# Kernel optimization log

Hardware: AMD Instinct MI355X
Metric: run time of the kernel (lower is better)

The kernel has to match this reference:

```python
import jax, jax.numpy as jnp
import numpy as np
from math import pi

FC_IN, FC_OUT = 64, 64
LABEL_NC = 35
B, C, H, W = 2, 64, 128, 128
EPS = 1e-5
SLOPE = 0.01  # torch leaky_relu default


def _pa(h, w):
    # absolute normalized coordinates, matches init_pos buffers
    xs = (jnp.arange(h, dtype=jnp.float32) / h) * 2.0 - 1.0
    ys = (jnp.arange(w, dtype=jnp.float32) / w) * 2.0 - 1.0
    px = jnp.broadcast_to(xs[:, None], (h, w))
    py = jnp.broadcast_to(ys[None, :], (h, w))
    return jnp.stack([px, py], 0)  # (2,h,w)


def _coords(h, w):
    # f0=3; while-loop runs once (f=3 -> f=1), so exactly 4 channels
    f = 3.0
    ang_x = 2.0 * pi * jnp.remainder(jnp.arange(w, dtype=jnp.float32), f) / f
    ang_y = 2.0 * pi * jnp.remainder(jnp.arange(h, dtype=jnp.float32), f) / f
    xcos = jnp.broadcast_to(jnp.cos(ang_x)[None, :], (h, w))
    xsin = jnp.broadcast_to(jnp.sin(ang_x)[None, :], (h, w))
    ycos = jnp.broadcast_to(jnp.cos(ang_y)[:, None], (h, w))
    ysin = jnp.broadcast_to(jnp.sin(ang_y)[:, None], (h, w))
    return jnp.stack([xcos, xsin, ycos, ysin], 0)  # (4,h,w)


def _nearest(t, h, w):
    # F.interpolate(mode='nearest') index map: floor(i*in/out)
    ih = jnp.arange(h) * t.shape[2] // h
    iw = jnp.arange(w) * t.shape[3] // w
    return t[:, :, ih][:, :, :, iw]


def setup_inputs() -> dict:
    key = jax.random.key(0)
    ks = jax.random.split(key, 7)
    return {
        "x": jax.random.normal(ks[0], (B, C, H, W), jnp.float32),
        "layout": jax.random.normal(ks[1], (B, LABEL_NC, H, W), jnp.float32),
        "pr": jax.random.normal(ks[2], (B, 2, H, W), jnp.float32),
        "conv_w": jax.random.normal(ks[3], (1, 10), jnp.float32) * 0.02,
        "conv_b": jnp.zeros((1,), jnp.float32),
        "W_table": jax.random.normal(ks[4], (LABEL_NC, FC_IN * FC_OUT), jnp.float32),
        "b_table": jax.random.normal(ks[5], (LABEL_NC, FC_OUT), jnp.float32) * 0.02,
        "pl": jax.random.normal(ks[6], (2, H, W), jnp.float32),
    }


def reference(x, layout, pr, conv_w, conv_b, W_table, b_table, pl):
    b, c, h, w = x.shape
    pa = jnp.broadcast_to(_pa(h, w)[None], (b, 2, h, w))
    plb = jnp.broadcast_to(pl[None], (b, 2, h, w))
    coords = jnp.broadcast_to(_coords(h, w)[None], (b, 4, h, w))
    prr = _nearest(pr, h, w)
    pos = jnp.concatenate([pa, plb, prr, coords], axis=1)  # (B,10,h,w)
    # 1x1 conv to a single channel, broadcast-added over C
    x = x + jnp.einsum('bchw,oc->bohw', pos, conv_w) + conv_b[None, :, None, None]
    # argmax-routed per-pixel affine params
    lay = _nearest(layout, h, w)
    arg = jnp.argmax(lay, axis=1)  # (B,h,w) int
    Wg = W_table[arg].reshape(b, h, w, FC_IN, FC_OUT)  # huge gathered tensor (as in original)
    bg = b_table[arg]  # (B,h,w,FC_OUT)
    xh = jnp.transpose(x, (0, 2, 3, 1))  # (B,h,w,C)
    y = jnp.einsum('bhwc,bhwco->bhwo', xh, Wg) + bg
    y = jnp.transpose(y, (0, 3, 1, 2))  # (B,FC_OUT,h,w)
    # instance norm (no affine, biased variance, eps=1e-5)
    mu = jnp.mean(y, axis=(2, 3), keepdims=True)
    var = jnp.var(y, axis=(2, 3), keepdims=True)
    y = (y - mu) * jax.lax.rsqrt(var + EPS)
    return jnp.where(y >= 0, y, SLOPE * y)
```

## Files before the change

kernel.cpp:

```cpp
#include <hip/hip_runtime.h>

#define HH 128
#define WW 128
#define NPIX (HH*WW)
#define NC 35
#define NB1 512
#define NWIN 16
#define NGB (NC*NWIN)
#define NG (2*NGB)

__global__ __launch_bounds__(256) void prep_kernel(
    const float* __restrict__ x, const float* __restrict__ layout,
    const float* __restrict__ pr, const float* __restrict__ cw,
    const float* __restrict__ cb, const float* __restrict__ pl,
    float* __restrict__ xt, int* __restrict__ argbuf)
{
    __shared__ float s_t[64*65];
    __shared__ float s_s[64];

    const int t  = threadIdx.x;
    const int bk = blockIdx.x;
    const int b  = bk >> 8;
    const int p0 = (bk & 255) << 6;
    const int h  = p0 >> 7;
    const int w0 = p0 & 127;

    const float4* x4 = (const float4*)x + (size_t)b*64*4096 + (p0 >> 2);
    #pragma unroll
    for (int k = 0; k < 4; ++k) {
        int f = k*256 + t;
        int c = f >> 4, i = f & 15;
        float4 q = x4[c*4096 + i];
        int base = c*65 + i*4;
        s_t[base+0]=q.x; s_t[base+1]=q.y; s_t[base+2]=q.z; s_t[base+3]=q.w;
    }

    if (t < 64) {
        int w = w0 + t;
        float pxv = (float)h * (2.0f/128.0f) - 1.0f;
        float pyv = (float)w * (2.0f/128.0f) - 1.0f;
        float pl0 = pl[h*WW + w];
        float pl1 = pl[NPIX + h*WW + w];
        float pr0 = pr[((b*2+0)*HH + h)*WW + w];
        float pr1 = pr[((b*2+1)*HH + h)*WW + w];
        int kx = w % 3, kyy = h % 3;
        const float C1 = -0.5f, S1 = 0.86602540378443864676f;
        float xcv = (kx==0)  ? 1.0f : C1;
        float xsv = (kx==0)  ? 0.0f : ((kx==1)  ? S1 : -S1);
        float ycv = (kyy==0) ? 1.0f : C1;
        float ysv = (kyy==0) ? 0.0f : ((kyy==1) ? S1 : -S1);
        s_s[t] = cb[0] + pxv*cw[0] + pyv*cw[1] + pl0*cw[2] + pl1*cw[3]
               + pr0*cw[4] + pr1*cw[5] + xcv*cw[6] + xsv*cw[7]
               + ycv*cw[8] + ysv*cw[9];
    } else if (t < 128) {
        int lane = t - 64;
        const float* lp = layout + (size_t)(b*NC)*NPIX + p0 + lane;
        float best = lp[0]; int bj = 0;
        #pragma unroll
        for (int c = 1; c < NC; ++c) {
            float v = lp[(size_t)c*NPIX];
            if (v > best) { best = v; bj = c; }
        }
        argbuf[b*NPIX + p0 + lane] = bj;
    }
    __syncthreads();

    float4* xt4 = (float4*)xt + ((size_t)b*NPIX + p0)*16;
    #pragma unroll
    for (int k = 0; k < 4; ++k) {
        int g = k*256 + t;
        int p = g >> 4, c4 = g & 15;
        float sp = s_s[p];
        float4 q;
        q.x = s_t[(c4*4+0)*65 + p] + sp;
        q.y = s_t[(c4*4+1)*65 + p] + sp;
        q.z = s_t[(c4*4+2)*65 + p] + sp;
        q.w = s_t[(c4*4+3)*65 + p] + sp;
        xt4[p*16 + c4] = q;
    }
}

__global__ __launch_bounds__(256) void gemm_kernel(
    const float* __restrict__ Wt, const float* __restrict__ bt,
    const float* __restrict__ xt, const int* __restrict__ argbuf,
    float* __restrict__ yt, float* __restrict__ psum, float* __restrict__ pss)
{
    const int g   = blockIdx.x;
    const int b   = g / NGB;
    const int rem = g % NGB;
    const int l   = rem >> 4;
    const int win = rem & (NWIN-1);
    const int t = threadIdx.x, wv = t >> 6, lane = t & 63;

    __shared__ int   s_list[1024];
    __shared__ int   s_n;
    __shared__ float s_x[64*64];
    __shared__ float s_red[4][64][2];

    if (t == 0) s_n = 0;
    __syncthreads();

    const int wpix = win*1024;
    #pragma unroll
    for (int j = 0; j < 4; ++j) {
        int idx = wv*256 + j*64 + lane;
        int a = argbuf[b*NPIX + wpix + idx];
        bool match = (a == l);
        unsigned long long mask = __ballot(match);
        int total = __popcll(mask);
        if (total) {
            int base = 0;
            if (lane == 0) base = atomicAdd(&s_n, total);
            base = __shfl(base, 0);
            if (match) {
                int rank = __popcll(mask & ((1ull << lane) - 1ull));
                s_list[base + rank] = wpix + idx;
            }
        }
    }

    float Wcol[64];
    const float* Wl = Wt + l*4096 + lane;
    #pragma unroll
    for (int c = 0; c < 64; ++c) Wcol[c] = Wl[c*64];
    float bias = bt[l*64 + lane];
    __syncthreads();
    const int m = s_n;

    float ssum = 0.f, sss = 0.f;
    for (int base0 = 0; base0 < m; base0 += 64) {
        int mm = min(64, m - base0);
        {
            int p = t >> 2, j = t & 3;
            if (p < mm) {
                const float4* r = (const float4*)xt + ((size_t)b*NPIX + s_list[base0+p])*16;
                #pragma unroll
                for (int k = 0; k < 4; ++k)
                    ((float4*)(s_x + p*64 + j*16))[k] = r[j*4 + k];
            }
        }
        __syncthreads();
        for (int i = wv; i < mm; i += 4) {
            const float4* xr = (const float4*)(s_x + i*64);
            float a0 = bias, a1 = 0.f, a2 = 0.f, a3 = 0.f;
            #pragma unroll
            for (int c4 = 0; c4 < 16; c4 += 4) {
                float4 q0 = xr[c4+0], q1 = xr[c4+1], q2 = xr[c4+2], q3 = xr[c4+3];
                a0 = fmaf(q0.x, Wcol[4*c4+ 0], a0); a0 = fmaf(q0.y, Wcol[4*c4+ 1], a0);
                a0 = fmaf(q0.z, Wcol[4*c4+ 2], a0); a0 = fmaf(q0.w, Wcol[4*c4+ 3], a0);
                a1 = fmaf(q1.x, Wcol[4*c4+ 4], a1); a1 = fmaf(q1.y, Wcol[4*c4+ 5], a1);
                a1 = fmaf(q1.z, Wcol[4*c4+ 6], a1); a1 = fmaf(q1.w, Wcol[4*c4+ 7], a1);
                a2 = fmaf(q2.x, Wcol[4*c4+ 8], a2); a2 = fmaf(q2.y, Wcol[4*c4+ 9], a2);
                a2 = fmaf(q2.z, Wcol[4*c4+10], a2); a2 = fmaf(q2.w, Wcol[4*c4+11], a2);
                a3 = fmaf(q3.x, Wcol[4*c4+12], a3); a3 = fmaf(q3.y, Wcol[4*c4+13], a3);
                a3 = fmaf(q3.z, Wcol[4*c4+14], a3); a3 = fmaf(q3.w, Wcol[4*c4+15], a3);
            }
            float acc = (a0 + a1) + (a2 + a3);
            yt[((size_t)b*NPIX + s_list[base0+i])*64 + lane] = acc;
            ssum += acc; sss += acc*acc;
        }
        __syncthreads();
    }

    s_red[wv][lane][0] = ssum;
    s_red[wv][lane][1] = sss;
    __syncthreads();
    if (wv == 0) {
        float S  = s_red[0][lane][0]+s_red[1][lane][0]+s_red[2][lane][0]+s_red[3][lane][0];
        float SS = s_red[0][lane][1]+s_red[1][lane][1]+s_red[2][lane][1]+s_red[3][lane][1];
        psum[g*64 + lane] = S;
        pss [g*64 + lane] = SS;
    }
}

__global__ __launch_bounds__(256) void stats_kernel(
    const float* __restrict__ psum, const float* __restrict__ pss,
    float* __restrict__ stats)
{
    __shared__ float red[256][2];
    const int e = blockIdx.x;
    const int b = e >> 6, o = e & 63;
    const int t = threadIdx.x;
    float S = 0.f, SS = 0.f;
    for (int gl = t; gl < NGB; gl += 256) {
        int g = b*NGB + gl;
        S  += psum[g*64 + o];
        SS += pss [g*64 + o];
    }
    red[t][0] = S; red[t][1] = SS;
    __syncthreads();
    #pragma unroll
    for (int s = 128; s > 0; s >>= 1) {
        if (t < s) { red[t][0] += red[t+s][0]; red[t][1] += red[t+s][1]; }
        __syncthreads();
    }
    if (t == 0) {
        const float invN = 1.0f/16384.0f;
        float mean = red[0][0] * invN;
        float var  = red[0][1] * invN - mean*mean;
        stats[e*2+0] = mean;
        stats[e*2+1] = rsqrtf(var + 1e-5f);
    }
}

__global__ __launch_bounds__(256) void norm_kernel(
    const float* __restrict__ yt, const float* __restrict__ stats,
    float* __restrict__ out)
{
    __shared__ float s_t[64*65];
    __shared__ float s_mean[64], s_rstd[64];

    const int t  = threadIdx.x;
    const int bk = blockIdx.x;
    const int b  = bk >> 8;
    const int p0 = (bk & 255) << 6;

    if (t < 64) {
        s_mean[t] = stats[(b*64+t)*2+0];
        s_rstd[t] = stats[(b*64+t)*2+1];
    }

    const float4* y4 = (const float4*)yt + ((size_t)b*NPIX + p0)*16;
    #pragma unroll
    for (int k = 0; k < 4; ++k) {
        int g = k*256 + t;
        int p = g >> 4, o4 = g & 15;
        float4 q = y4[p*16 + o4];
        int base = (o4*4)*65 + p;
        s_t[base]     = q.x;
        s_t[base+65]  = q.y;
        s_t[base+130] = q.z;
        s_t[base+195] = q.w;
    }
    __syncthreads();

    const int p = t & 63, og = (t >> 6) * 16;
    float* op = out + ((size_t)b*64 + og)*NPIX + p0 + p;
    #pragma unroll
    for (int kk = 0; kk < 16; ++kk) {
        int o = og + kk;
        float v = (s_t[o*65 + p] - s_mean[o]) * s_rstd[o];
        op[(size_t)kk*NPIX] = (v >= 0.f) ? v : 0.01f*v;
    }
}

extern "C" void kernel_launch(void* const* d_in, const int* in_sizes, int n_in,
                              void* d_out, int out_size, void* d_ws, size_t ws_size,
                              hipStream_t stream) {
    const float* x      = (const float*)d_in[0];
    const float* layout = (const float*)d_in[1];
    const float* pr     = (const float*)d_in[2];
    const float* cw     = (const float*)d_in[3];
    const float* cb     = (const float*)d_in[4];
    const float* Wt     = (const float*)d_in[5];
    const float* bt     = (const float*)d_in[6];
    const float* pl     = (const float*)d_in[7];
    float* out = (float*)d_out;

    char* ws = (char*)d_ws;
    size_t off = 0;
    float* xt     = (float*)(ws + off); off += (size_t)2*NPIX*64*4;
    float* yt     = (float*)(ws + off); off += (size_t)2*NPIX*64*4;
    int*   argbuf = (int*)  (ws + off); off += (size_t)2*NPIX*4;
    float* psum   = (float*)(ws + off); off += (size_t)NG*64*4;
    float* pss    = (float*)(ws + off); off += (size_t)NG*64*4;
    float* stats  = (float*)(ws + off); off += 128*2*4;

    prep_kernel <<<NB1, 256, 0, stream>>>(x, layout, pr, cw, cb, pl, xt, argbuf);
    gemm_kernel <<<NG,  256, 0, stream>>>(Wt, bt, xt, argbuf, yt, psum, pss);
    stats_kernel<<<128, 256, 0, stream>>>(psum, pss, stats);
    norm_kernel <<<NB1, 256, 0, stream>>>(yt, stats, out);
}
```

Baseline: 103.4 us.

## Fold stats reduction into gemm via atomics and widen pixel windows

Removes the separate stats kernel: each gemm block atomically adds its per-channel sum and sum of squares into a small zeroed buffer, and the norm kernel derives mean and rstd itself. Block 0 of the prep kernel zeroes the buffer. Windows are doubled to 2048 pixels, so half as many gemm blocks are launched and each one loads its weight column once for more pixels. This saves one launch and the partial-sum traffic, at the cost of float-atomic nondeterminism and fewer, larger blocks that may balance load less evenly.

```diff
diff --git a/kernel.cpp b/kernel.cpp
--- a/kernel.cpp
+++ b/kernel.cpp
@@ -5,7 +5,8 @@
 #define NPIX (HH*WW)
 #define NC 35
 #define NB1 512
-#define NWIN 16
+#define NWIN 8
+#define WPX 2048
 #define NGB (NC*NWIN)
 #define NG (2*NGB)
 
@@ -13,7 +14,7 @@
     const float* __restrict__ x, const float* __restrict__ layout,
     const float* __restrict__ pr, const float* __restrict__ cw,
     const float* __restrict__ cb, const float* __restrict__ pl,
-    float* __restrict__ xt, int* __restrict__ argbuf)
+    float* __restrict__ xt, int* __restrict__ argbuf, float* __restrict__ sums)
 {
     __shared__ float s_t[64*65];
     __shared__ float s_s[64];
@@ -24,6 +25,8 @@
     const int p0 = (bk & 255) << 6;
     const int h  = p0 >> 7;
     const int w0 = p0 & 127;
+
+    if (bk == 0) sums[t] = 0.f;
 
     const float4* x4 = (const float4*)x + (size_t)b*64*4096 + (p0 >> 2);
     #pragma unroll
@@ -83,16 +86,16 @@
 __global__ __launch_bounds__(256) void gemm_kernel(
     const float* __restrict__ Wt, const float* __restrict__ bt,
     const float* __restrict__ xt, const int* __restrict__ argbuf,
-    float* __restrict__ yt, float* __restrict__ psum, float* __restrict__ pss)
+    float* __restrict__ yt, float* __restrict__ sums)
 {
     const int g   = blockIdx.x;
     const int b   = g / NGB;
     const int rem = g % NGB;
-    const int l   = rem >> 4;
+    const int l   = rem >> 3;
     const int win = rem & (NWIN-1);
     const int t = threadIdx.x, wv = t >> 6, lane = t & 63;
 
-    __shared__ int   s_list[1024];
+    __shared__ int   s_list[WPX];
     __shared__ int   s_n;
     __shared__ float s_x[64*64];
     __shared__ float s_red[4][64][2];
@@ -100,10 +103,10 @@
     if (t == 0) s_n = 0;
     __syncthreads();
 
-    const int wpix = win*1024;
-    #pragma unroll
-    for (int j = 0; j < 4; ++j) {
-        int idx = wv*256 + j*64 + lane;
+    const int wpix = win*WPX;
+    #pragma unroll
+    for (int j = 0; j < WPX/256; ++j) {
+        int idx = wv*(WPX/4) + j*64 + lane;
         int a = argbuf[b*NPIX + wpix + idx];
         bool match = (a == l);
         unsigned long long mask = __ballot(match);
@@ -168,43 +171,15 @@
     if (wv == 0) {
         float S  = s_red[0][lane][0]+s_red[1][lane][0]+s_red[2][lane][0]+s_red[3][lane][0];
         float SS = s_red[0][lane][1]+s_red[1][lane][1]+s_red[2][lane][1]+s_red[3][lane][1];
-        psum[g*64 + lane] = S;
-        pss [g*64 + lane] = SS;
-    }
-}
-
-__global__ __launch_bounds__(256) void stats_kernel(
-    const float* __restrict__ psum, const float* __restrict__ pss,
-    float* __restrict__ stats)
-{
-    __shared__ float red[256][2];
-    const int e = blockIdx.x;
-    const int b = e >> 6, o = e & 63;
-    const int t = threadIdx.x;
-    float S = 0.f, SS = 0.f;
-    for (int gl = t; gl < NGB; gl += 256) {
-        int g = b*NGB + gl;
-        S  += psum[g*64 + o];
-        SS += pss [g*64 + o];
-    }
-    red[t][0] = S; red[t][1] = SS;
-    __syncthreads();
-    #pragma unroll
-    for (int s = 128; s > 0; s >>= 1) {
-        if (t < s) { red[t][0] += red[t+s][0]; red[t][1] += red[t+s][1]; }
-        __syncthreads();
-    }
-    if (t == 0) {
-        const float invN = 1.0f/16384.0f;
-        float mean = red[0][0] * invN;
-        float var  = red[0][1] * invN - mean*mean;
-        stats[e*2+0] = mean;
-        stats[e*2+1] = rsqrtf(var + 1e-5f);
+        if (S != 0.f || SS != 0.f) {
+            atomicAdd(&sums[(b*64+lane)*2+0], S);
+            atomicAdd(&sums[(b*64+lane)*2+1], SS);
+        }
     }
 }
 
 __global__ __launch_bounds__(256) void norm_kernel(
-    const float* __restrict__ yt, const float* __restrict__ stats,
+    const float* __restrict__ yt, const float* __restrict__ sums,
     float* __restrict__ out)
 {
     __shared__ float s_t[64*65];
@@ -216,8 +191,13 @@
     const int p0 = (bk & 255) << 6;
 
     if (t < 64) {
-        s_mean[t] = stats[(b*64+t)*2+0];
-        s_rstd[t] = stats[(b*64+t)*2+1];
+        float S  = sums[(b*64+t)*2+0];
+        float SS = sums[(b*64+t)*2+1];
+        const float invN = 1.0f/16384.0f;
+        float mean = S * invN;
+        float var  = SS * invN - mean*mean;
+        s_mean[t] = mean;
+        s_rstd[t] = rsqrtf(var + 1e-5f);
     }
 
     const float4* y4 = (const float4*)yt + ((size_t)b*NPIX + p0)*16;
@@ -262,12 +242,9 @@
     float* xt     = (float*)(ws + off); off += (size_t)2*NPIX*64*4;
     float* yt     = (float*)(ws + off); off += (size_t)2*NPIX*64*4;
     int*   argbuf = (int*)  (ws + off); off += (size_t)2*NPIX*4;
-    float* psum   = (float*)(ws + off); off += (size_t)NG*64*4;
-    float* pss    = (float*)(ws + off); off += (size_t)NG*64*4;
-    float* stats  = (float*)(ws + off); off += 128*2*4;
-
-    prep_kernel <<<NB1, 256, 0, stream>>>(x, layout, pr, cw, cb, pl, xt, argbuf);
-    gemm_kernel <<<NG,  256, 0, stream>>>(Wt, bt, xt, argbuf, yt, psum, pss);
-    stats_kernel<<<128, 256, 0, stream>>>(psum, pss, stats);
-    norm_kernel <<<NB1, 256, 0, stream>>>(yt, stats, out);
-}
+    float* sums   = (float*)(ws + off); off += 256*4;
+
+    prep_kernel <<<NB1, 256, 0, stream>>>(x, layout, pr, cw, cb, pl, xt, argbuf, sums);
+    gemm_kernel <<<NG,  256, 0, stream>>>(Wt, bt, xt, argbuf, yt, sums);
+    norm_kernel <<<NB1, 256, 0, stream>>>(yt, sums, out);
+}
```

New measurement: 111.5 us. 1.08x slower.
